# Optimization experiments

Measured on AMD Instinct MI355X. Metric: run time of the kernel, lower is better.

The kernel has to match this reference:

```python
import jax, jax.numpy as jnp
import numpy as np

# SMPL kinematic tree (24 joints); parent[0] = -1 (root)
PARENT = [-1, 0, 0, 0, 1, 2, 3, 4, 5, 6, 7, 8, 9, 9, 9, 12, 13, 14, 16, 17, 18, 19, 20, 21]
J = len(PARENT)  # 24


def _ancestor_matrix(parent):
    # A[j, k] = 1 if offset k contributes to joint j (k on path root->j, excluding root)
    n = len(parent)
    A = np.zeros((n, n), dtype=np.float32)
    for j in range(1, n):
        k = j
        while k > 0:
            A[j, k] = 1.0
            k = parent[k]
    return A

ANC = jnp.asarray(_ancestor_matrix(PARENT))  # [J, J]


def setup_inputs() -> dict:
    key = jax.random.key(0)
    k0, k1, k2 = jax.random.split(key, 3)
    B, D, H = 131072, 256, 512
    out_dim = (J - 1) * 4
    z = jax.random.normal(k0, (B, D), jnp.float32)
    W1 = jax.random.normal(k1, (D, H), jnp.float32) / np.float32(np.sqrt(D))
    b1 = jnp.zeros((H,), jnp.float32)
    W2 = jax.random.normal(k2, (H, out_dim), jnp.float32) / np.float32(np.sqrt(H))
    b2 = jnp.zeros((out_dim,), jnp.float32)
    return {"z": z, "W1": W1, "b1": b1, "W2": W2, "b2": b2}


def reference(z, W1, b1, W2, b2):
    B = z.shape[0]
    h = jax.nn.silu(z @ W1 + b1)                      # [B, 512]
    raw = (h @ W2 + b2).reshape(B, J - 1, 4)          # [B, J-1, 4]
    dir_raw = raw[..., :3]                            # [B, J-1, 3]
    len_raw = raw[..., 3]                             # [B, J-1]
    # F.normalize(dim=-1, eps=1e-6): x / max(||x||, eps)
    norm = jnp.linalg.norm(dir_raw, axis=-1, keepdims=True)
    direction = dir_raw / jnp.maximum(norm, 1e-6)
    length = jax.nn.softplus(len_raw)                 # [B, J-1]
    offset_non_root = direction * length[..., None]
    offsets = jnp.concatenate(
        [jnp.zeros((B, 1, 3), z.dtype), offset_non_root], axis=1
    )  # [B, J, 3]
    # Forward kinematics: joints[j] = sum of offsets along ancestor chain.
    # The sequential per-joint loop collapses to one matmul with the
    # precomputed ancestor incidence matrix (same math, depth-parallel).
    joints = jnp.einsum('jk,bkc->bjc', ANC, offsets)  # [B, J, 3]
    return (joints, offsets, length)
```

## Files before the change

### kernel.cpp

```cpp
#include <hip/hip_runtime.h>
#include <math.h>

typedef _Float16 half8 __attribute__((ext_vector_type(8)));
typedef float floatx4 __attribute__((ext_vector_type(4)));

#define DD 256
#define HH 512
#define OC 92
#define NJ 24
#define BM 128
#define NCHUNK 16
#define W2P_OFF 131072
#define FLAG_OFF 196608
#define FCAP 16384
#define BUF_BYTES 24576

__constant__ int c_parent[NJ] = {-1,0,0,0,1,2,3,4,5,6,7,8,9,9,9,12,13,14,16,17,18,19,20,21};


__global__ __launch_bounds__(256)
void prep(const float* __restrict__ W1, const float* __restrict__ W2,
          _Float16* __restrict__ ws, int* __restrict__ flags) {
    int t = blockIdx.x * 256 + threadIdx.x;
    if (t == 0) flags[0] = 0;
    if (t < 16384) {
        int lane = t & 63;
        int cfrag = (t >> 6) & 1;
        int ks = (t >> 7) & 7;
        int ckI = t >> 10;
        int c = ckI * 32 + cfrag * 16 + (lane & 15);
        int kb = ks * 32 + 4 * (lane >> 4);
        half8 v;
        #pragma unroll
        for (int j = 0; j < 8; ++j) {
            int k = kb + (j & 3) + 16 * (j >> 2);
            v[j] = (_Float16)W1[k * HH + c];
        }
        *(half8*)(ws + t * 8) = v;
    } else {
        int u = t - 16384;
        int lane = u & 63;
        int s = (u >> 6) & 7;
        int ck = u >> 9;
        half8 v;
        if (s < 6) {
            int c = s * 16 + (lane & 15);
            int kb = ck * 32 + 4 * (lane >> 4);
            #pragma unroll
            for (int j = 0; j < 8; ++j) {
                int k = kb + (j & 3) + 16 * (j >> 2);
                v[j] = (c < OC) ? (_Float16)W2[k * OC + c] : (_Float16)0.0f;
            }
        } else {
            #pragma unroll
            for (int j = 0; j < 8; ++j) v[j] = (_Float16)0.0f;
        }
        *(half8*)(ws + W2P_OFF + ck * 4096 + (s * 64 + lane) * 8) = v;
    }
}

__global__ __launch_bounds__(256)
__attribute__((amdgpu_waves_per_eu(2, 3)))
void fused_main(const float* __restrict__ z, const _Float16* __restrict__ wsp,
                const float* __restrict__ b1, const float* __restrict__ b2,
                float* __restrict__ out, long long Btot, int* __restrict__ flags)
{
    __shared__ __align__(16) char smem[2 * BUF_BYTES + 2048 + 384];
    float* b1f = (float*)(smem + 2 * BUF_BYTES);
    float* b2f = (float*)(smem + 2 * BUF_BYTES + 2048);
    const int tid = threadIdx.x;
    const int w   = tid >> 6;
    const int l   = tid & 63;
    const int l15 = l & 15;
    const int l4  = l >> 4;

    const long long R0  = (long long)blockIdx.x * BM;
    const long long R0w = R0 + w * 32;

#define STAGE(ck_, dstbuf_) do {                                                             \
    const char* s1g_ = (const char*)wsp + (size_t)(ck_) * 16384;                             \
    const char* s2g_ = (const char*)(wsp + W2P_OFF) + (size_t)(ck_) * 8192;                  \
    _Pragma("unroll")                                                                        \
    for (int i_ = 0; i_ < 6; ++i_) {                                                         \
        int g_ = w * 6 + i_;                                                                 \
        const char* src_ = (g_ < 16) ? (s1g_ + g_ * 1024) : (s2g_ + (g_ - 16) * 1024);       \
        __builtin_amdgcn_global_load_lds(                                                    \
            (const __attribute__((address_space(1))) void*)(src_ + l * 16),                  \
            (__attribute__((address_space(3))) void*)((dstbuf_) + g_ * 1024), 16, 0, 0);     \
    }                                                                                        \
} while (0)

#define COMPUTE_CHUNK(bufc_, ck_) do {                                                       \
    const _Float16* s1_ = (const _Float16*)(bufc_);                                          \
    const _Float16* s2_ = (const _Float16*)((bufc_) + 16384);                                \
    floatx4 vb1_[2];                                                                         \
    vb1_[0] = *(const floatx4*)(b1f + (ck_) * 32 + 4 * l4);                                  \
    vb1_[1] = *(const floatx4*)(b1f + (ck_) * 32 + 16 + 4 * l4);                             \
    floatx4 acc1_[2][2];                                                                     \
    acc1_[0][0] = (floatx4)0.0f; acc1_[0][1] = (floatx4)0.0f;                                \
    acc1_[1][0] = (floatx4)0.0f; acc1_[1][1] = (floatx4)0.0f;                                \
    _Pragma("unroll")                                                                        \
    for (int ks_ = 0; ks_ < 8; ++ks_) {                                                      \
        _Pragma("unroll")                                                                    \
        for (int cf_ = 0; cf_ < 2; ++cf_) {                                                  \
            half8 bh_ = *(const half8*)(s1_ + ((ks_ * 2 + cf_) * 64 + l) * 8);               \
            acc1_[0][cf_] = __builtin_amdgcn_mfma_f32_16x16x32_f16(bh_, zh[0][ks_], acc1_[0][cf_], 0, 0, 0); \
            acc1_[1][cf_] = __builtin_amdgcn_mfma_f32_16x16x32_f16(bh_, zh[1][ks_], acc1_[1][cf_], 0, 0, 0); \
        }                                                                                    \
    }                                                                                        \
    half8 ah_[2];                                                                            \
    _Pragma("unroll")                                                                        \
    for (int at_ = 0; at_ < 2; ++at_) {                                                      \
        _Pragma("unroll")                                                                    \
        for (int cf_ = 0; cf_ < 2; ++cf_) {                                                  \
            _Pragma("unroll")                                                                \
            for (int i_ = 0; i_ < 4; ++i_) {                                                 \
                float a_ = acc1_[at_][cf_][i_] + vb1_[cf_][i_];                              \
                float hv_ = a_ * __builtin_amdgcn_rcpf(1.0f + __expf(-a_));                  \
                ah_[at_][i_ | (cf_ << 2)] = (_Float16)hv_;                                   \
            }                                                                                \
        }                                                                                    \
    }                                                                                        \
    _Pragma("unroll")                                                                        \
    for (int cf_ = 0; cf_ < 6; ++cf_) {                                                      \
        half8 w2h_ = *(const half8*)(s2_ + (cf_ * 64 + l) * 8);                              \
        a2[0][cf_] = __builtin_amdgcn_mfma_f32_16x16x32_f16(w2h_, ah_[0], a2[0][cf_], 0, 0, 0); \
        a2[1][cf_] = __builtin_amdgcn_mfma_f32_16x16x32_f16(w2h_, ah_[1], a2[1][cf_], 0, 0, 0); \
    }                                                                                        \
} while (0)

    STAGE(0, smem);
    if (tid < 128) *(floatx4*)(b1f + tid * 4) = *(const floatx4*)(b1 + tid * 4);
    if (tid >= 128 && tid < 224) { int c = tid - 128; b2f[c] = (c < OC) ? b2[c] : 0.0f; }

    half8 zh[2][8];
    #pragma unroll
    for (int at = 0; at < 2; ++at) {
        const float* zrow = z + (R0w + (long long)(at * 16 + l15)) * DD;
        #pragma unroll
        for (int ks = 0; ks < 8; ++ks) {
            const float* p = zrow + ks * 32 + l4 * 4;
            floatx4 va = *(const floatx4*)p;
            floatx4 vb = *(const floatx4*)(p + 16);
            half8 th;
            th[0] = (_Float16)va[0]; th[1] = (_Float16)va[1];
            th[2] = (_Float16)va[2]; th[3] = (_Float16)va[3];
            th[4] = (_Float16)vb[0]; th[5] = (_Float16)vb[1];
            th[6] = (_Float16)vb[2]; th[7] = (_Float16)vb[3];
            zh[at][ks] = th;
        }
    }

    floatx4 a2[2][6];
    #pragma unroll
    for (int at = 0; at < 2; ++at)
        #pragma unroll
        for (int i = 0; i < 6; ++i) a2[at][i] = (floatx4)0.0f;

    __syncthreads();

    #pragma unroll 1
    for (int t = 0; t < 8; ++t) {
        STAGE(2 * t + 1, smem + BUF_BYTES);
        COMPUTE_CHUNK(smem, 2 * t);
        asm volatile("s_waitcnt vmcnt(0)" ::: "memory");
        __builtin_amdgcn_s_barrier();
        if (t < 7) STAGE(2 * t + 2, smem);
        COMPUTE_CHUNK(smem + BUF_BYTES, 2 * t + 1);
        asm volatile("s_waitcnt vmcnt(0)" ::: "memory");
        __builtin_amdgcn_s_barrier();
    }

    float* s_off = (float*)smem + w * 3040;
    float* s_len = s_off + 2304;

    #pragma unroll
    for (int at = 0; at < 2; ++at) {
        const int r = at * 16 + l15;
        #pragma unroll
        for (int cf = 0; cf < 6; ++cf) {
            const int j = 4 * cf + l4;
            if (j < NJ - 1) {
                float x  = a2[at][cf][0] + b2f[4 * j + 0];
                float y  = a2[at][cf][1] + b2f[4 * j + 1];
                float zz = a2[at][cf][2] + b2f[4 * j + 2];
                float lr = a2[at][cf][3] + b2f[4 * j + 3];
                float nrm = sqrtf(x * x + y * y + zz * zz);
                float inv = __builtin_amdgcn_rcpf(fmaxf(nrm, 1e-6f));
                float len = fmaxf(lr, 0.0f) + __logf(1.0f + __expf(-fabsf(lr)));
                if (len > 12.0f * nrm) {
                    int fi = atomicAdd(&flags[0], 1);
                    if (fi < FCAP) flags[1 + fi] = (int)(R0w + r);
                }
                s_off[r * 72 + 3 * (j + 1) + 0] = x * inv * len;
                s_off[r * 72 + 3 * (j + 1) + 1] = y * inv * len;
                s_off[r * 72 + 3 * (j + 1) + 2] = zz * inv * len;
                s_len[r * 23 + j] = len;
            }
        }
    }
    if (l < 32) {
        s_off[l * 72 + 0] = 0.0f;
        s_off[l * 72 + 1] = 0.0f;
        s_off[l * 72 + 2] = 0.0f;
    }
    __syncthreads();

    float* joints  = out;
    float* offsets = out + Btot * (NJ * 3);
    float* length  = out + 2 * Btot * (NJ * 3);

    {
        float* gdst = offsets + R0w * (NJ * 3);
        #pragma unroll
        for (int t4 = 0; t4 < 9; ++t4) {
            int idx = (t4 * 64 + l) * 4;
            *(float4*)(gdst + idx) = *(float4*)(s_off + idx);
        }
    }
    {
        float* gdst = length + R0w * (NJ - 1);
        for (int t4 = l; t4 < 184; t4 += 64) {
            *(float4*)(gdst + t4 * 4) = *(float4*)(s_len + t4 * 4);
        }
    }
    for (int task = l; task < 32 * NJ; task += 64) {
        int r = task / NJ;
        int j = task - r * NJ;
        float jx = 0.0f, jy = 0.0f, jz = 0.0f;
        int k = j;
        while (k > 0) {
            jx += s_off[r * 72 + 3 * k + 0];
            jy += s_off[r * 72 + 3 * k + 1];
            jz += s_off[r * 72 + 3 * k + 2];
            k = c_parent[k];
        }
        long long base = (R0w + r) * (NJ * 3) + j * 3;
        joints[base + 0] = jx;
        joints[base + 1] = jy;
        joints[base + 2] = jz;
    }
#undef STAGE
#undef COMPUTE_CHUNK
}

__global__ __launch_bounds__(256)
void fixup(const float* __restrict__ z, const float* __restrict__ W1,
           const float* __restrict__ b1, const float* __restrict__ W2,
           const float* __restrict__ b2, float* __restrict__ out,
           long long Btot, const int* __restrict__ flags)
{
    __shared__ float z_s[DD];
    __shared__ float h_s[HH];
    __shared__ float raw_s[96];
    __shared__ float off_s[72];
    int n = flags[0];
    if (n > FCAP) n = FCAP;
    if ((int)blockIdx.x >= n) return;
    const int tid = threadIdx.x;
    const long long row = flags[1 + blockIdx.x];

    float* joints  = out;
    float* offsets = out + Btot * (NJ * 3);
    float* length  = out + 2 * Btot * (NJ * 3);

    z_s[tid] = z[row * DD + tid];
    __syncthreads();
    for (int c = tid; c < HH; c += 256) {
        float acc = b1[c];
        for (int k = 0; k < DD; ++k) acc = fmaf(z_s[k], W1[k * HH + c], acc);
        h_s[c] = acc / (1.0f + expf(-acc));
    }
    __syncthreads();
    if (tid < OC) {
        float acc = b2[tid];
        for (int k = 0; k < HH; ++k) acc = fmaf(h_s[k], W2[k * OC + tid], acc);
        raw_s[tid] = acc;
    }
    __syncthreads();
    if (tid < NJ - 1) {
        int j = tid;
        float x  = raw_s[4 * j + 0];
        float y  = raw_s[4 * j + 1];
        float zz = raw_s[4 * j + 2];
        float lr = raw_s[4 * j + 3];
        float nrm = sqrtf(x * x + y * y + zz * zz);
        float inv = 1.0f / fmaxf(nrm, 1e-6f);
        float len = fmaxf(lr, 0.0f) + log1pf(expf(-fabsf(lr)));
        off_s[3 * (j + 1) + 0] = x * inv * len;
        off_s[3 * (j + 1) + 1] = y * inv * len;
        off_s[3 * (j + 1) + 2] = zz * inv * len;
        length[row * (NJ - 1) + j] = len;
    }
    if (tid < 3) off_s[tid] = 0.0f;
    __syncthreads();
    if (tid < NJ) {
        int j = tid;
        float jx = 0.0f, jy = 0.0f, jz = 0.0f;
        int k = j;
        while (k > 0) {
            jx += off_s[3 * k + 0];
            jy += off_s[3 * k + 1];
            jz += off_s[3 * k + 2];
            k = c_parent[k];
        }
        joints[row * (NJ * 3) + j * 3 + 0] = jx;
        joints[row * (NJ * 3) + j * 3 + 1] = jy;
        joints[row * (NJ * 3) + j * 3 + 2] = jz;
    }
    if (tid < NJ * 3) offsets[row * (NJ * 3) + tid] = off_s[tid];
}

extern "C" void kernel_launch(void* const* d_in, const int* in_sizes, int n_in,
                              void* d_out, int out_size, void* d_ws, size_t ws_size,
                              hipStream_t stream) {
    const float* z  = (const float*)d_in[0];
    const float* W1 = (const float*)d_in[1];
    const float* b1 = (const float*)d_in[2];
    const float* W2 = (const float*)d_in[3];
    const float* b2 = (const float*)d_in[4];
    float* out = (float*)d_out;
    _Float16* ws = (_Float16*)d_ws;
    int* flags = (int*)(ws + FLAG_OFF);

    const long long Btot = (long long)in_sizes[0] / DD;

    prep<<<96, 256, 0, stream>>>(W1, W2, ws, flags);
    fused_main<<<(int)(Btot / BM), 256, 0, stream>>>(z, ws, b1, b2, out, Btot, flags);
    fixup<<<4096, 256, 0, stream>>>(z, W1, b1, W2, b2, out, Btot, flags);
}
```

Measured before the change: 147.8 us.

## Halve rows per block, load W2 fragments from global, raise occupancy

Each block now handles 64 rows (16 per wave) instead of 128, halving the z fragments and accumulators kept in registers. W2 is no longer staged through LDS; each wave reads its W2 fragments straight from global memory (likely L2-resident), which shrinks the staging buffers. The occupancy hint goes from 2-3 to 4 waves per EU. The trade-off is half as much reuse of each staged W1 chunk per block, twice as many blocks, and more global traffic for W2.

```diff
diff --git a/kernel.cpp b/kernel.cpp
--- a/kernel.cpp
+++ b/kernel.cpp
@@ -8,12 +8,12 @@
 #define HH 512
 #define OC 92
 #define NJ 24
-#define BM 128
+#define BM 64
 #define NCHUNK 16
-#define W2P_OFF 131072
-#define FLAG_OFF 196608
+#define W2_OFF 131072
+#define FLAG_OFF 180224
 #define FCAP 16384
-#define BUF_BYTES 24576
+#define BUF_BYTES 16384
 
 __constant__ int c_parent[NJ] = {-1,0,0,0,1,2,3,4,5,6,7,8,9,9,9,12,13,14,16,17,18,19,20,21};
 
@@ -37,95 +37,85 @@
             v[j] = (_Float16)W1[k * HH + c];
         }
         *(half8*)(ws + t * 8) = v;
-    } else {
+    } else if (t < 16384 + 6144) {
         int u = t - 16384;
         int lane = u & 63;
-        int s = (u >> 6) & 7;
-        int ck = u >> 9;
+        int rest = u >> 6;
+        int cfrag = rest % 6;
+        int ckI = rest / 6;
+        int c = cfrag * 16 + (lane & 15);
+        int kb = ckI * 32 + 4 * (lane >> 4);
         half8 v;
-        if (s < 6) {
-            int c = s * 16 + (lane & 15);
-            int kb = ck * 32 + 4 * (lane >> 4);
-            #pragma unroll
-            for (int j = 0; j < 8; ++j) {
-                int k = kb + (j & 3) + 16 * (j >> 2);
-                v[j] = (c < OC) ? (_Float16)W2[k * OC + c] : (_Float16)0.0f;
-            }
-        } else {
-            #pragma unroll
-            for (int j = 0; j < 8; ++j) v[j] = (_Float16)0.0f;
-        }
-        *(half8*)(ws + W2P_OFF + ck * 4096 + (s * 64 + lane) * 8) = v;
+        #pragma unroll
+        for (int j = 0; j < 8; ++j) {
+            int k = kb + (j & 3) + 16 * (j >> 2);
+            v[j] = (c < OC) ? (_Float16)W2[k * OC + c] : (_Float16)0.0f;
+        }
+        *(half8*)(ws + W2_OFF + (ckI * 6 + cfrag) * 512 + lane * 8) = v;
     }
 }
 
 __global__ __launch_bounds__(256)
-__attribute__((amdgpu_waves_per_eu(2, 3)))
+__attribute__((amdgpu_waves_per_eu(4)))
 void fused_main(const float* __restrict__ z, const _Float16* __restrict__ wsp,
                 const float* __restrict__ b1, const float* __restrict__ b2,
                 float* __restrict__ out, long long Btot, int* __restrict__ flags)
 {
-    __shared__ __align__(16) char smem[2 * BUF_BYTES + 2048 + 384];
-    float* b1f = (float*)(smem + 2 * BUF_BYTES);
-    float* b2f = (float*)(smem + 2 * BUF_BYTES + 2048);
+    __shared__ __align__(16) char smem[35200];
+    float* b1f = (float*)(smem + 32768);
+    float* b2f = (float*)(smem + 34816);
     const int tid = threadIdx.x;
     const int w   = tid >> 6;
     const int l   = tid & 63;
     const int l15 = l & 15;
     const int l4  = l >> 4;
 
-    const long long R0  = (long long)blockIdx.x * BM;
-    const long long R0w = R0 + w * 32;
+    const long long R0w = (long long)blockIdx.x * BM + w * 16;
 
 #define STAGE(ck_, dstbuf_) do {                                                             \
     const char* s1g_ = (const char*)wsp + (size_t)(ck_) * 16384;                             \
-    const char* s2g_ = (const char*)(wsp + W2P_OFF) + (size_t)(ck_) * 8192;                  \
-    _Pragma("unroll")                                                                        \
-    for (int i_ = 0; i_ < 6; ++i_) {                                                         \
-        int g_ = w * 6 + i_;                                                                 \
-        const char* src_ = (g_ < 16) ? (s1g_ + g_ * 1024) : (s2g_ + (g_ - 16) * 1024);       \
+    _Pragma("unroll")                                                                        \
+    for (int i_ = 0; i_ < 4; ++i_) {                                                         \
+        int g_ = w * 4 + i_;                                                                 \
         __builtin_amdgcn_global_load_lds(                                                    \
-            (const __attribute__((address_space(1))) void*)(src_ + l * 16),                  \
+            (const __attribute__((address_space(1))) void*)(s1g_ + g_ * 1024 + l * 16),      \
             (__attribute__((address_space(3))) void*)((dstbuf_) + g_ * 1024), 16, 0, 0);     \
     }                                                                                        \
 } while (0)
 
+#define MF(a_, b_, c_) __builtin_amdgcn_mfma_f32_16x16x32_f16((a_), (b_), (c_), 0, 0, 0)
+
 #define COMPUTE_CHUNK(bufc_, ck_) do {                                                       \
     const _Float16* s1_ = (const _Float16*)(bufc_);                                          \
-    const _Float16* s2_ = (const _Float16*)((bufc_) + 16384);                                \
-    floatx4 vb1_[2];                                                                         \
-    vb1_[0] = *(const floatx4*)(b1f + (ck_) * 32 + 4 * l4);                                  \
-    vb1_[1] = *(const floatx4*)(b1f + (ck_) * 32 + 16 + 4 * l4);                             \
-    floatx4 acc1_[2][2];                                                                     \
-    acc1_[0][0] = (floatx4)0.0f; acc1_[0][1] = (floatx4)0.0f;                                \
-    acc1_[1][0] = (floatx4)0.0f; acc1_[1][1] = (floatx4)0.0f;                                \
+    const _Float16* p2_ = wsp + W2_OFF + (ck_) * 3072 + l * 8;                               \
+    half8 w2f_[6];                                                                           \
+    _Pragma("unroll")                                                                        \
+    for (int cf_ = 0; cf_ < 6; ++cf_) w2f_[cf_] = *(const half8*)(p2_ + cf_ * 512);          \
+    floatx4 acc1_[2];                                                                        \
+    acc1_[0] = (floatx4)0.0f; acc1_[1] = (floatx4)0.0f;                                      \
     _Pragma("unroll")                                                                        \
     for (int ks_ = 0; ks_ < 8; ++ks_) {                                                      \
         _Pragma("unroll")                                                                    \
         for (int cf_ = 0; cf_ < 2; ++cf_) {                                                  \
             half8 bh_ = *(const half8*)(s1_ + ((ks_ * 2 + cf_) * 64 + l) * 8);               \
-            acc1_[0][cf_] = __builtin_amdgcn_mfma_f32_16x16x32_f16(bh_, zh[0][ks_], acc1_[0][cf_], 0, 0, 0); \
-            acc1_[1][cf_] = __builtin_amdgcn_mfma_f32_16x16x32_f16(bh_, zh[1][ks_], acc1_[1][cf_], 0, 0, 0); \
+            acc1_[cf_] = MF(bh_, zh[ks_], acc1_[cf_]);                                       \
         }                                                                                    \
     }                                                                                        \
-    half8 ah_[2];                                                                            \
-    _Pragma("unroll")                                                                        \
-    for (int at_ = 0; at_ < 2; ++at_) {                                                      \
+    floatx4 vb1a_ = *(const floatx4*)(b1f + (ck_) * 32 + 4 * l4);                            \
+    floatx4 vb1b_ = *(const floatx4*)(b1f + (ck_) * 32 + 16 + 4 * l4);                       \
+    half8 ah_;                                                                               \
+    _Pragma("unroll")                                                                        \
+    for (int cf_ = 0; cf_ < 2; ++cf_) {                                                      \
         _Pragma("unroll")                                                                    \
-        for (int cf_ = 0; cf_ < 2; ++cf_) {                                                  \
-            _Pragma("unroll")                                                                \
-            for (int i_ = 0; i_ < 4; ++i_) {                                                 \
-                float a_ = acc1_[at_][cf_][i_] + vb1_[cf_][i_];                              \
-                float hv_ = a_ * __builtin_amdgcn_rcpf(1.0f + __expf(-a_));                  \
-                ah_[at_][i_ | (cf_ << 2)] = (_Float16)hv_;                                   \
-            }                                                                                \
+        for (int i_ = 0; i_ < 4; ++i_) {                                                     \
+            float a_ = acc1_[cf_][i_] + (cf_ ? vb1b_[i_] : vb1a_[i_]);                       \
+            float hv_ = a_ * __builtin_amdgcn_rcpf(1.0f + __expf(-a_));                      \
+            ah_[i_ | (cf_ << 2)] = (_Float16)hv_;                                            \
         }                                                                                    \
     }                                                                                        \
     _Pragma("unroll")                                                                        \
     for (int cf_ = 0; cf_ < 6; ++cf_) {                                                      \
-        half8 w2h_ = *(const half8*)(s2_ + (cf_ * 64 + l) * 8);                              \
-        a2[0][cf_] = __builtin_amdgcn_mfma_f32_16x16x32_f16(w2h_, ah_[0], a2[0][cf_], 0, 0, 0); \
-        a2[1][cf_] = __builtin_amdgcn_mfma_f32_16x16x32_f16(w2h_, ah_[1], a2[1][cf_], 0, 0, 0); \
+        a2[cf_] = MF(w2f_[cf_], ah_, a2[cf_]);                                               \
     }                                                                                        \
 } while (0)
 
@@ -133,10 +123,9 @@
     if (tid < 128) *(floatx4*)(b1f + tid * 4) = *(const floatx4*)(b1 + tid * 4);
     if (tid >= 128 && tid < 224) { int c = tid - 128; b2f[c] = (c < OC) ? b2[c] : 0.0f; }
 
-    half8 zh[2][8];
-    #pragma unroll
-    for (int at = 0; at < 2; ++at) {
-        const float* zrow = z + (R0w + (long long)(at * 16 + l15)) * DD;
+    half8 zh[8];
+    {
+        const float* zrow = z + (R0w + l15) * DD;
         #pragma unroll
         for (int ks = 0; ks < 8; ++ks) {
             const float* p = zrow + ks * 32 + l4 * 4;
@@ -147,15 +136,13 @@
             th[2] = (_Float16)va[2]; th[3] = (_Float16)va[3];
             th[4] = (_Float16)vb[0]; th[5] = (_Float16)vb[1];
             th[6] = (_Float16)vb[2]; th[7] = (_Float16)vb[3];
-            zh[at][ks] = th;
-        }
-    }
-
-    floatx4 a2[2][6];
+            zh[ks] = th;
+        }
+    }
+
+    floatx4 a2[6];
     #pragma unroll
-    for (int at = 0; at < 2; ++at)
-        #pragma unroll
-        for (int i = 0; i < 6; ++i) a2[at][i] = (floatx4)0.0f;
+    for (int i = 0; i < 6; ++i) a2[i] = (floatx4)0.0f;
 
     __syncthreads();
 
@@ -171,20 +158,22 @@
         __builtin_amdgcn_s_barrier();
     }
 
-    float* s_off = (float*)smem + w * 3040;
-    float* s_len = s_off + 2304;
-
-    #pragma unroll
-    for (int at = 0; at < 2; ++at) {
-        const int r = at * 16 + l15;
+    float* joints  = out;
+    float* offsets = out + Btot * (NJ * 3);
+    float* length  = out + 2 * Btot * (NJ * 3);
+
+    {
+        float* s_off = (float*)(smem + w * 6080);
+        float* s_len = s_off + 1152;
+        const int r = l15;
         #pragma unroll
         for (int cf = 0; cf < 6; ++cf) {
             const int j = 4 * cf + l4;
             if (j < NJ - 1) {
-                float x  = a2[at][cf][0] + b2f[4 * j + 0];
-                float y  = a2[at][cf][1] + b2f[4 * j + 1];
-                float zz = a2[at][cf][2] + b2f[4 * j + 2];
-                float lr = a2[at][cf][3] + b2f[4 * j + 3];
+                float x  = a2[cf][0] + b2f[4 * j + 0];
+                float y  = a2[cf][1] + b2f[4 * j + 1];
+                float zz = a2[cf][2] + b2f[4 * j + 2];
+                float lr = a2[cf][3] + b2f[4 * j + 3];
                 float nrm = sqrtf(x * x + y * y + zz * zz);
                 float inv = __builtin_amdgcn_rcpf(fmaxf(nrm, 1e-6f));
                 float len = fmaxf(lr, 0.0f) + __logf(1.0f + __expf(-fabsf(lr)));
@@ -198,50 +187,43 @@
                 s_len[r * 23 + j] = len;
             }
         }
-    }
-    if (l < 32) {
-        s_off[l * 72 + 0] = 0.0f;
-        s_off[l * 72 + 1] = 0.0f;
-        s_off[l * 72 + 2] = 0.0f;
-    }
-    __syncthreads();
-
-    float* joints  = out;
-    float* offsets = out + Btot * (NJ * 3);
-    float* length  = out + 2 * Btot * (NJ * 3);
-
-    {
-        float* gdst = offsets + R0w * (NJ * 3);
-        #pragma unroll
-        for (int t4 = 0; t4 < 9; ++t4) {
-            int idx = (t4 * 64 + l) * 4;
-            *(float4*)(gdst + idx) = *(float4*)(s_off + idx);
-        }
-    }
-    {
-        float* gdst = length + R0w * (NJ - 1);
-        for (int t4 = l; t4 < 184; t4 += 64) {
-            *(float4*)(gdst + t4 * 4) = *(float4*)(s_len + t4 * 4);
-        }
-    }
-    for (int task = l; task < 32 * NJ; task += 64) {
-        int r = task / NJ;
-        int j = task - r * NJ;
-        float jx = 0.0f, jy = 0.0f, jz = 0.0f;
-        int k = j;
-        while (k > 0) {
-            jx += s_off[r * 72 + 3 * k + 0];
-            jy += s_off[r * 72 + 3 * k + 1];
-            jz += s_off[r * 72 + 3 * k + 2];
-            k = c_parent[k];
-        }
-        long long base = (R0w + r) * (NJ * 3) + j * 3;
-        joints[base + 0] = jx;
-        joints[base + 1] = jy;
-        joints[base + 2] = jz;
+        if (l < 16) {
+            s_off[l * 72 + 0] = 0.0f;
+            s_off[l * 72 + 1] = 0.0f;
+            s_off[l * 72 + 2] = 0.0f;
+        }
+        __syncthreads();
+
+        {
+            float* gdst = offsets + R0w * (NJ * 3);
+            for (int t4 = l; t4 < 288; t4 += 64)
+                *(float4*)(gdst + t4 * 4) = *(float4*)(s_off + t4 * 4);
+        }
+        {
+            float* gdst = length + R0w * (NJ - 1);
+            for (int t4 = l; t4 < 92; t4 += 64)
+                *(float4*)(gdst + t4 * 4) = *(float4*)(s_len + t4 * 4);
+        }
+        for (int task = l; task < 16 * NJ; task += 64) {
+            int rr = task / NJ;
+            int j = task - rr * NJ;
+            float jx = 0.0f, jy = 0.0f, jz = 0.0f;
+            int k = j;
+            while (k > 0) {
+                jx += s_off[rr * 72 + 3 * k + 0];
+                jy += s_off[rr * 72 + 3 * k + 1];
+                jz += s_off[rr * 72 + 3 * k + 2];
+                k = c_parent[k];
+            }
+            long long base = (R0w + rr) * (NJ * 3) + j * 3;
+            joints[base + 0] = jx;
+            joints[base + 1] = jy;
+            joints[base + 2] = jz;
+        }
     }
 #undef STAGE
 #undef COMPUTE_CHUNK
+#undef MF
 }
 
 __global__ __launch_bounds__(256)
@@ -325,7 +307,7 @@
 
     const long long Btot = (long long)in_sizes[0] / DD;
 
-    prep<<<96, 256, 0, stream>>>(W1, W2, ws, flags);
+    prep<<<88, 256, 0, stream>>>(W1, W2, ws, flags);
     fused_main<<<(int)(Btot / BM), 256, 0, stream>>>(z, ws, b1, b2, out, Btot, flags);
     fixup<<<4096, 256, 0, stream>>>(z, W1, b1, W2, b2, out, Btot, flags);
 }
```

Result: faster. 143.6 us, median of 3 (-2.8%).
